# Kernel optimization log

Measured on AMD Instinct MI355X. Metric: run time of the kernel, lower is better.

Reference implementation:

```python
import jax, jax.numpy as jnp
import numpy as np

B, T, H, NH, V = 2, 2048, 512, 8, 32000
HD = H // NH  # head dim

def setup_inputs() -> dict:
    key = jax.random.key(0)
    ks = jax.random.split(key, 15)
    s = 0.02
    rn = lambda k, shp: (jax.random.normal(k, shp, dtype=jnp.float32) * s)
    return {
        "ixs": jax.random.randint(ks[0], (B, T), 0, V, dtype=jnp.int32),
        "tok_emb": rn(ks[1], (V, H)),
        "pos_emb": rn(ks[2], (1, T, H)),
        "W_prj": rn(ks[3], (H, H)),
        "Wq": rn(ks[4], (H, H)), "bq": rn(ks[5], (H,)),
        "Wk": rn(ks[6], (H, H)), "bk": rn(ks[7], (H,)),
        "Wv": rn(ks[8], (H, H)), "bv": rn(ks[9], (H,)),
        "W1": rn(ks[10], (H, H)), "b1": rn(ks[11], (H,)),
        "W2": rn(ks[12], (V, H)), "b2": rn(ks[13], (V,)),
    }

def reference(ixs, tok_emb, pos_emb, W_prj, Wq, bq, Wk, bk, Wv, bv, W1, b1, W2, b2):
    b, t = ixs.shape
    # embeddings + projection (prj1 has no bias)
    x = tok_emb[ixs] + pos_emb[:, :t, :]          # [B,T,H]
    x = x @ W_prj.T                                # [B,T,H]
    # multi-head causal attention; NOTE: scale uses full hidden dim (allH**0.5)
    def heads(W, bias):
        return (x @ W.T + bias).reshape(b, t, NH, HD).transpose(0, 2, 1, 3)  # [B,nH,T,HD]
    q, k, v = heads(Wq, bq), heads(Wk, bk), heads(Wv, bv)
    att = jnp.einsum('bhqd,bhkd->bhqk', q, k) / (H ** 0.5)  # [B,nH,T,T]
    causal = jnp.tril(jnp.ones((t, t), dtype=bool))
    att = jnp.where(causal, att, -jnp.inf)
    w = jax.nn.softmax(att, axis=-1)
    y = jnp.einsum('bhqk,bhkd->bhqd', w, v)        # [B,nH,T,HD]
    y = y.transpose(0, 2, 1, 3).reshape(b, t, H)   # [B,T,H]
    # MLP: Linear->ReLU->Linear->ReLU (final ReLU per original loop condition)
    h1 = jax.nn.relu(y @ W1.T + b1)                # [B,T,H]
    out = jax.nn.relu(h1 @ W2.T + b2)              # [B,T,V]
    return out
```

## Files before the change

kernel.cpp:

```cpp
#include <hip/hip_runtime.h>
#include <stdint.h>
#include <stddef.h>

#define TSEQ   2048
#define HDIM   512
#define NHEADS 8
#define HEADD  64
#define NVOCAB 32000
#define NROWS  4096

typedef unsigned short ushort_t;
typedef __bf16 bf16x8 __attribute__((ext_vector_type(8)));
typedef float  f32x4  __attribute__((ext_vector_type(4)));
typedef unsigned short us8 __attribute__((ext_vector_type(8)));
typedef unsigned short us4 __attribute__((ext_vector_type(4)));
typedef unsigned short us2 __attribute__((ext_vector_type(2)));

__device__ __forceinline__ ushort_t f2bf(float f){
  union { float f; unsigned int u; } v; v.f = f;
  unsigned int u = v.u;
  u += 0x7FFFu + ((u >> 16) & 1u);
  return (ushort_t)(u >> 16);
}

__device__ __forceinline__ void gload_lds16(const ushort_t* g, ushort_t* l){
  __builtin_amdgcn_global_load_lds(
      (const __attribute__((address_space(1))) void*)g,
      (__attribute__((address_space(3))) void*)l, 16, 0, 0);
}

__global__ void cvt_bf16_kernel(const float* __restrict__ src,
                                ushort_t* __restrict__ dst, int n4){
  int stride = gridDim.x * blockDim.x;
  for (int i = blockIdx.x * blockDim.x + threadIdx.x; i < n4; i += stride){
    float4 f = ((const float4*)src)[i];
    us4 o;
    o[0] = f2bf(f.x); o[1] = f2bf(f.y); o[2] = f2bf(f.z); o[3] = f2bf(f.w);
    ((us4*)dst)[i] = o;
  }
}

__global__ void embed_kernel(const int* __restrict__ ixs, const float* __restrict__ tok,
                             const float* __restrict__ pos, ushort_t* __restrict__ x0){
  const int r = blockIdx.x;
  const int t = r & (TSEQ - 1);
  const int ix = ixs[r];
  const int j = threadIdx.x;
  const float2 a = ((const float2*)(tok + (size_t)ix * HDIM))[j];
  const float2 p = ((const float2*)(pos + (size_t)t * HDIM))[j];
  us2 o; o[0] = f2bf(a.x + p.x); o[1] = f2bf(a.y + p.y);
  *(us2*)(x0 + (size_t)r * HDIM + j * 2) = o;
}

template<int HAS_BIAS, int RELU, int OUT_F32>
__global__ __launch_bounds__(256) void gemm_bt_kernel(
    const ushort_t* __restrict__ A, const ushort_t* __restrict__ W,
    const float* __restrict__ bias, void* __restrict__ outp,
    int M, int N, int K)
{
  __shared__ ushort_t As[128 * 64];
  __shared__ ushort_t Bs[128 * 64];
  const int tid  = threadIdx.x;
  const int wave = tid >> 6;
  const int lane = tid & 63;
  const int lr   = lane & 15;
  const int lg   = lane >> 4;
  const int nbx  = N >> 7;
  const int bx   = blockIdx.x % nbx;
  const int by   = blockIdx.x / nbx;
  const int row0 = by << 7;
  const int col0 = bx << 7;
  const int wr   = wave >> 1, wc = wave & 1;

  f32x4 acc[4][4];
#pragma unroll
  for (int m = 0; m < 4; m++)
#pragma unroll
    for (int n = 0; n < 4; n++) acc[m][n] = (f32x4){0.f, 0.f, 0.f, 0.f};

  const int e    = tid * 8;
  const int srow = e >> 6;
  const int scol = e & 63;
  const ushort_t* gA = A + (size_t)(row0 + srow) * K + scol;
  const ushort_t* gB = W + (size_t)(col0 + srow) * K + scol;
  const int ldsbase = wave * 512;

  for (int kt = 0; kt < K; kt += 64){
#pragma unroll
    for (int p = 0; p < 4; p++){
      gload_lds16(gA + (size_t)(p * 32) * K + kt, &As[p * 2048 + ldsbase]);
      gload_lds16(gB + (size_t)(p * 32) * K + kt, &Bs[p * 2048 + ldsbase]);
    }
    __syncthreads();
#pragma unroll
    for (int kk = 0; kk < 64; kk += 32){
      bf16x8 af[4], bfr[4];
#pragma unroll
      for (int m = 0; m < 4; m++)
        af[m] = __builtin_bit_cast(bf16x8,
            *(const us8*)&As[(wr * 64 + m * 16 + lr) * 64 + kk + lg * 8]);
#pragma unroll
      for (int n = 0; n < 4; n++)
        bfr[n] = __builtin_bit_cast(bf16x8,
            *(const us8*)&Bs[(wc * 64 + n * 16 + lr) * 64 + kk + lg * 8]);
#pragma unroll
      for (int m = 0; m < 4; m++)
#pragma unroll
        for (int n = 0; n < 4; n++)
          acc[m][n] = __builtin_amdgcn_mfma_f32_16x16x32_bf16(af[m], bfr[n], acc[m][n], 0, 0, 0);
    }
    __syncthreads();
  }

#pragma unroll
  for (int n = 0; n < 4; n++){
    const int col = col0 + wc * 64 + n * 16 + lr;
    float bv = 0.f;
    if (HAS_BIAS) bv = bias[col];
#pragma unroll
    for (int m = 0; m < 4; m++){
      const int rowb = row0 + wr * 64 + m * 16 + lg * 4;
#pragma unroll
      for (int r = 0; r < 4; r++){
        float vv = acc[m][n][r] + bv;
        if (RELU) vv = fmaxf(vv, 0.f);
        const size_t o = (size_t)(rowb + r) * N + col;
        if (OUT_F32) ((float*)outp)[o] = vv;
        else         ((ushort_t*)outp)[o] = f2bf(vv);
      }
    }
  }
}

__global__ __launch_bounds__(256) void attn_kernel(
    const ushort_t* __restrict__ qkv, ushort_t* __restrict__ y)
{
  __shared__ ushort_t Ks[64 * 64];
  __shared__ ushort_t Vt[64 * 64];
  __shared__ ushort_t Ps[4][16 * 64];
  const int qt   = blockIdx.x;
  const int hb   = blockIdx.y;
  const int b    = hb >> 3;
  const int h    = hb & 7;
  const int tid  = threadIdx.x;
  const int wave = tid >> 6, lane = tid & 63;
  const int lr   = lane & 15, lg = lane >> 4;
  const int ld   = 3 * HDIM;
  const size_t rowbase = (size_t)b * TSEQ;
  const ushort_t* kb = qkv + HDIM;
  const ushort_t* vb = qkv + 2 * HDIM;

  const int qrow = qt * 64 + wave * 16 + lr;
  const ushort_t* qp = qkv + (rowbase + qrow) * ld + h * HEADD;
  bf16x8 qf[2];
  qf[0] = __builtin_bit_cast(bf16x8, *(const us8*)&qp[lg * 8]);
  qf[1] = __builtin_bit_cast(bf16x8, *(const us8*)&qp[32 + lg * 8]);

  float m_run[4], l_run[4];
  f32x4 acc_o[4];
#pragma unroll
  for (int i = 0; i < 4; i++){ m_run[i] = -1e30f; l_run[i] = 0.f; acc_o[i] = (f32x4){0,0,0,0}; }

  const int e    = tid * 8;
  const int srow = e >> 6;
  const int scol = e & 63;
  const float scale = 0.04419417382415922f;

  for (int kt = 0; kt <= qt; ++kt){
    const ushort_t* gK = kb + (rowbase + kt * 64 + srow) * ld + h * HEADD + scol;
    gload_lds16(gK,                     &Ks[wave * 512]);
    gload_lds16(gK + (size_t)32 * ld,   &Ks[2048 + wave * 512]);
    const ushort_t* gV = vb + (rowbase + kt * 64 + srow) * ld + h * HEADD + scol;
    us8 v0 = *(const us8*)gV;
    us8 v1 = *(const us8*)(gV + (size_t)32 * ld);
#pragma unroll
    for (int j = 0; j < 8; j++){
      Vt[(scol + j) * 64 + srow]      = v0[j];
      Vt[(scol + j) * 64 + srow + 32] = v1[j];
    }
    __syncthreads();

    f32x4 s[4];
#pragma unroll
    for (int n = 0; n < 4; n++){
      s[n] = (f32x4){0, 0, 0, 0};
#pragma unroll
      for (int ks = 0; ks < 2; ks++){
        bf16x8 kf = __builtin_bit_cast(bf16x8,
            *(const us8*)&Ks[(n * 16 + lr) * 64 + ks * 32 + lg * 8]);
        s[n] = __builtin_amdgcn_mfma_f32_16x16x32_bf16(qf[ks], kf, s[n], 0, 0, 0);
      }
    }

    float sv[4][4];
    float tmax[4] = {-1e30f, -1e30f, -1e30f, -1e30f};
    const bool diag = (kt == qt);
#pragma unroll
    for (int n = 0; n < 4; n++)
#pragma unroll
      for (int r = 0; r < 4; r++){
        float x = s[n][r] * scale;
        if (diag && (n * 16 + lr) > (wave * 16 + lg * 4 + r)) x = -1e30f;
        sv[n][r] = x;
        tmax[r] = fmaxf(tmax[r], x);
      }
#pragma unroll
    for (int off = 1; off < 16; off <<= 1)
#pragma unroll
      for (int r = 0; r < 4; r++) tmax[r] = fmaxf(tmax[r], __shfl_xor(tmax[r], off));

    float alpha[4], psum[4];
#pragma unroll
    for (int r = 0; r < 4; r++){
      float mn = fmaxf(m_run[r], tmax[r]);
      alpha[r] = __expf(m_run[r] - mn);
      m_run[r] = mn;
      psum[r] = 0.f;
    }
    float p[4][4];
#pragma unroll
    for (int n = 0; n < 4; n++)
#pragma unroll
      for (int r = 0; r < 4; r++){ p[n][r] = __expf(sv[n][r] - m_run[r]); psum[r] += p[n][r]; }
#pragma unroll
    for (int off = 1; off < 16; off <<= 1)
#pragma unroll
      for (int r = 0; r < 4; r++) psum[r] += __shfl_xor(psum[r], off);
#pragma unroll
    for (int r = 0; r < 4; r++) l_run[r] = l_run[r] * alpha[r] + psum[r];
#pragma unroll
    for (int nd = 0; nd < 4; nd++)
#pragma unroll
      for (int r = 0; r < 4; r++) acc_o[nd][r] *= alpha[r];

#pragma unroll
    for (int n = 0; n < 4; n++)
#pragma unroll
      for (int r = 0; r < 4; r++)
        Ps[wave][(lg * 4 + r) * 64 + n * 16 + lr] = f2bf(p[n][r]);
    asm volatile("s_waitcnt lgkmcnt(0)" ::: "memory");
    bf16x8 pa[2];
    pa[0] = __builtin_bit_cast(bf16x8, *(const us8*)&Ps[wave][lr * 64 + lg * 8]);
    pa[1] = __builtin_bit_cast(bf16x8, *(const us8*)&Ps[wave][lr * 64 + 32 + lg * 8]);
#pragma unroll
    for (int nd = 0; nd < 4; nd++)
#pragma unroll
      for (int ks = 0; ks < 2; ks++){
        bf16x8 vf = __builtin_bit_cast(bf16x8,
            *(const us8*)&Vt[(nd * 16 + lr) * 64 + ks * 32 + lg * 8]);
        acc_o[nd] = __builtin_amdgcn_mfma_f32_16x16x32_bf16(pa[ks], vf, acc_o[nd], 0, 0, 0);
      }
    __syncthreads();
  }

  float inv[4];
#pragma unroll
  for (int r = 0; r < 4; r++) inv[r] = 1.f / l_run[r];
#pragma unroll
  for (int nd = 0; nd < 4; nd++)
#pragma unroll
    for (int r = 0; r < 4; r++){
      const int row_t = qt * 64 + wave * 16 + lg * 4 + r;
      y[(rowbase + row_t) * HDIM + h * HEADD + nd * 16 + lr] = f2bf(acc_o[nd][r] * inv[r]);
    }
}

extern "C" void kernel_launch(void* const* d_in, const int* in_sizes, int n_in,
                              void* d_out, int out_size, void* d_ws, size_t ws_size,
                              hipStream_t stream)
{
  const int*   ixs  = (const int*)  d_in[0];
  const float* tok  = (const float*)d_in[1];
  const float* pos  = (const float*)d_in[2];
  const float* Wprj = (const float*)d_in[3];
  const float* Wq   = (const float*)d_in[4];
  const float* bq_  = (const float*)d_in[5];
  const float* Wk   = (const float*)d_in[6];
  const float* bk_  = (const float*)d_in[7];
  const float* Wv   = (const float*)d_in[8];
  const float* bv_  = (const float*)d_in[9];
  const float* W1   = (const float*)d_in[10];
  const float* b1_  = (const float*)d_in[11];
  const float* W2   = (const float*)d_in[12];
  const float* b2_  = (const float*)d_in[13];
  float* out = (float*)d_out;

  ushort_t* ws    = (ushort_t*)d_ws;
  ushort_t* x0    = ws;
  ushort_t* x1    = x0    + 2097152;
  ushort_t* qkv   = x1    + 2097152;
  ushort_t* yb    = qkv   + 6291456;
  ushort_t* h1b   = yb    + 2097152;
  ushort_t* wprjb = h1b   + 2097152;
  ushort_t* wqkvb = wprjb + 262144;
  ushort_t* w1b   = wqkvb + 786432;
  ushort_t* w2b   = w1b   + 262144;
  float*    bqkv  = (float*)(w2b + 16384000);

  auto cvtN = [&](const float* s, ushort_t* d, int n){
    int n4 = n >> 2;
    int blocks = (n4 + 255) >> 8; if (blocks > 2048) blocks = 2048;
    cvt_bf16_kernel<<<blocks, 256, 0, stream>>>(s, d, n4);
  };
  cvtN(Wprj, wprjb, 262144);
  cvtN(Wq,   wqkvb,          262144);
  cvtN(Wk,   wqkvb + 262144, 262144);
  cvtN(Wv,   wqkvb + 524288, 262144);
  cvtN(W1,   w1b, 262144);
  cvtN(W2,   w2b, 16384000);
  hipMemcpyAsync(bqkv,        bq_, 512 * 4, hipMemcpyDeviceToDevice, stream);
  hipMemcpyAsync(bqkv + 512,  bk_, 512 * 4, hipMemcpyDeviceToDevice, stream);
  hipMemcpyAsync(bqkv + 1024, bv_, 512 * 4, hipMemcpyDeviceToDevice, stream);

  embed_kernel<<<NROWS, 256, 0, stream>>>(ixs, tok, pos, x0);

  gemm_bt_kernel<0,0,0><<<32 * 4,   256, 0, stream>>>(x0,  wprjb, nullptr, x1,  NROWS, 512,   512);
  gemm_bt_kernel<1,0,0><<<32 * 12,  256, 0, stream>>>(x1,  wqkvb, bqkv,    qkv, NROWS, 1536,  512);
  attn_kernel<<<dim3(32, 16), 256, 0, stream>>>(qkv, yb);
  gemm_bt_kernel<1,1,0><<<32 * 4,   256, 0, stream>>>(yb,  w1b,   b1_,     h1b, NROWS, 512,   512);
  gemm_bt_kernel<1,1,1><<<32 * 250, 256, 0, stream>>>(h1b, w2b,   b2_,     out, NROWS, NVOCAB, 512);
}
```

Baseline: 464.3 us.

## Fuse weight conversions and bias copies into one kernel; reorder GEMM tile mapping

Replaces six separate fp32→bf16 conversion launches and three device-to-device bias memcpys with a single grid-stride kernel that picks its source by index range. This is meant to cut launch and memcpy overhead before the main pipeline. The GEMM block index mapping also changes from row-major to column-major over output tiles, so consecutive blocks share the same weight tile, which changes L2 reuse patterns, mainly for the large vocab GEMM.

```diff
diff --git a/kernel.cpp b/kernel.cpp
--- a/kernel.cpp
+++ b/kernel.cpp
@@ -29,14 +29,36 @@
       (__attribute__((address_space(3))) void*)l, 16, 0, 0);
 }
 
-__global__ void cvt_bf16_kernel(const float* __restrict__ src,
-                                ushort_t* __restrict__ dst, int n4){
+#define CVT_N4   4423680
+#define CVT_TOT  4424064
+__global__ void cvt_all_kernel(const float* __restrict__ Wprj, const float* __restrict__ Wq,
+                               const float* __restrict__ Wk,   const float* __restrict__ Wv,
+                               const float* __restrict__ W1,   const float* __restrict__ W2,
+                               const float* __restrict__ bq,   const float* __restrict__ bk,
+                               const float* __restrict__ bv,
+                               ushort_t* __restrict__ wdst, float* __restrict__ bqkv){
   int stride = gridDim.x * blockDim.x;
-  for (int i = blockIdx.x * blockDim.x + threadIdx.x; i < n4; i += stride){
-    float4 f = ((const float4*)src)[i];
-    us4 o;
-    o[0] = f2bf(f.x); o[1] = f2bf(f.y); o[2] = f2bf(f.z); o[3] = f2bf(f.w);
-    ((us4*)dst)[i] = o;
+  for (int i = blockIdx.x * blockDim.x + threadIdx.x; i < CVT_TOT; i += stride){
+    if (i < CVT_N4){
+      const float* src; int j;
+      if (i < 327680){
+        int w = i >> 16;
+        j = i & 65535;
+        src = (w == 0) ? Wprj : (w == 1) ? Wq : (w == 2) ? Wk : (w == 3) ? Wv : W1;
+      } else {
+        j = i - 327680;
+        src = W2;
+      }
+      float4 f = ((const float4*)src)[j];
+      us4 o;
+      o[0] = f2bf(f.x); o[1] = f2bf(f.y); o[2] = f2bf(f.z); o[3] = f2bf(f.w);
+      ((us4*)wdst)[i] = o;
+    } else {
+      int j = i - CVT_N4;
+      const float* src = (j < 128) ? bq : (j < 256) ? bk : bv;
+      int jj = j & 127;
+      ((float4*)bqkv)[j] = ((const float4*)src)[jj];
+    }
   }
 }
 
@@ -65,9 +87,9 @@
   const int lane = tid & 63;
   const int lr   = lane & 15;
   const int lg   = lane >> 4;
-  const int nbx  = N >> 7;
-  const int bx   = blockIdx.x % nbx;
-  const int by   = blockIdx.x / nbx;
+  const int nby  = M >> 7;
+  const int by   = blockIdx.x % nby;
+  const int bx   = blockIdx.x / nby;
   const int row0 = by << 7;
   const int col0 = bx << 7;
   const int wr   = wave >> 1, wc = wave & 1;
@@ -297,20 +319,8 @@
   ushort_t* w2b   = w1b   + 262144;
   float*    bqkv  = (float*)(w2b + 16384000);
 
-  auto cvtN = [&](const float* s, ushort_t* d, int n){
-    int n4 = n >> 2;
-    int blocks = (n4 + 255) >> 8; if (blocks > 2048) blocks = 2048;
-    cvt_bf16_kernel<<<blocks, 256, 0, stream>>>(s, d, n4);
-  };
-  cvtN(Wprj, wprjb, 262144);
-  cvtN(Wq,   wqkvb,          262144);
-  cvtN(Wk,   wqkvb + 262144, 262144);
-  cvtN(Wv,   wqkvb + 524288, 262144);
-  cvtN(W1,   w1b, 262144);
-  cvtN(W2,   w2b, 16384000);
-  hipMemcpyAsync(bqkv,        bq_, 512 * 4, hipMemcpyDeviceToDevice, stream);
-  hipMemcpyAsync(bqkv + 512,  bk_, 512 * 4, hipMemcpyDeviceToDevice, stream);
-  hipMemcpyAsync(bqkv + 1024, bv_, 512 * 4, hipMemcpyDeviceToDevice, stream);
+  cvt_all_kernel<<<2048, 256, 0, stream>>>(Wprj, Wq, Wk, Wv, W1, W2,
+                                           bq_, bk_, bv_, wprjb, bqkv);
 
   embed_kernel<<<NROWS, 256, 0, stream>>>(ixs, tok, pos, x0);
 
```

After: 476.5 us. 2.6% more time.
